# Optimization experiments

Hardware: AMD Instinct MI355X
Metric: run time of the kernel (lower is better)

Reference implementation:

```python
import jax, jax.numpy as jnp
import numpy as np

N, E, IN, HID, OUT = 40000, 640000, 128, 512, 256


def setup_inputs() -> dict:
    key = jax.random.key(0)
    ks = jax.random.split(key, 8)
    x = jax.random.normal(ks[0], (N, IN), dtype=jnp.float32)
    edge_index = jax.random.randint(ks[1], (2, E), 0, N, dtype=jnp.int64)
    # SAGEConv params: lin_l (applied to aggregated neighbors, with bias),
    # lin_r (applied to root nodes, no bias) -- PyG defaults.
    def lin(k, fin, fout):
        return jax.random.normal(k, (fin, fout), dtype=jnp.float32) / np.sqrt(fin)
    return {
        "x": x,
        "edge_index": edge_index,
        "W1l": lin(ks[2], IN, HID),
        "b1": jnp.zeros((HID,), jnp.float32),
        "W1r": lin(ks[3], IN, HID),
        "W2l": lin(ks[4], HID, OUT),
        "b2": jnp.zeros((OUT,), jnp.float32),
        "W2r": lin(ks[5], HID, OUT),
    }


def _sage_conv(x, src, dst, Wl, b, Wr):
    n = x.shape[0]
    # gather messages from source nodes, mean-aggregate at destination
    msg = x[src]                                            # [E, F]
    agg = jax.ops.segment_sum(msg, dst, num_segments=n)     # [N, F]
    cnt = jax.ops.segment_sum(jnp.ones((src.shape[0],), x.dtype), dst,
                              num_segments=n)               # [N]
    agg = agg / jnp.maximum(cnt, 1.0)[:, None]
    # out = lin_l(mean_neighbors) + lin_r(x)
    return agg @ Wl + b + x @ Wr


def reference(x, edge_index, W1l, b1, W1r, W2l, b2, W2r):
    src, dst = edge_index[0], edge_index[1]
    h = jax.nn.relu(_sage_conv(x, src, dst, W1l, b1, W1r))
    return _sage_conv(h, src, dst, W2l, b2, W2r)
```

## Files before the change

kernel.cpp:

```cpp
#include <hip/hip_runtime.h>


#define N_NODES 40000
#define N_EDGES 640000
#define F_IN 128
#define F_HID 512
#define F_OUT 256
#define NB_SCAN 157

typedef unsigned short ushort_t;
typedef __attribute__((ext_vector_type(8))) short bf16x8;
typedef __attribute__((ext_vector_type(4))) float floatx4;

__device__ __forceinline__ ushort_t f2bf(float f) {
  union { float f; unsigned int u; } x; x.f = f;
  unsigned int r = (x.u + 0x7FFFu + ((x.u >> 16) & 1u)) >> 16;
  return (ushort_t)r;
}
__device__ __forceinline__ float bf2f(ushort_t u) {
  union { unsigned int u; float f; } x; x.u = ((unsigned int)u) << 16;
  return x.f;
}

__global__ void scanA_kernel(const int* __restrict__ deg, int* __restrict__ bsum) {
  __shared__ int sdata[256];
  int i = blockIdx.x * 256 + threadIdx.x;
  sdata[threadIdx.x] = (i < N_NODES) ? deg[i] : 0;
  __syncthreads();
  #pragma unroll
  for (int off = 128; off > 0; off >>= 1) {
    if (threadIdx.x < off) sdata[threadIdx.x] += sdata[threadIdx.x + off];
    __syncthreads();
  }
  if (threadIdx.x == 0) bsum[blockIdx.x] = sdata[0];
}

__global__ void scanB_kernel(const int* __restrict__ bsum, int* __restrict__ boff) {
  __shared__ int buf[2][256];
  int tid = threadIdx.x;
  int v = (tid < NB_SCAN) ? bsum[tid] : 0;
  buf[0][tid] = v;
  __syncthreads();
  int cur = 0;
  #pragma unroll
  for (int off = 1; off < 256; off <<= 1) {
    int val = buf[cur][tid];
    if (tid >= off) val += buf[cur][tid - off];
    buf[cur ^ 1][tid] = val;
    __syncthreads();
    cur ^= 1;
  }
  if (tid < NB_SCAN) boff[tid] = buf[cur][tid] - v;
}

__global__ void scanC_kernel(const int* __restrict__ deg, const int* __restrict__ boff,
                             int* __restrict__ rowptr, int* __restrict__ cursor) {
  __shared__ int buf[2][256];
  int tid = threadIdx.x;
  int i = blockIdx.x * 256 + tid;
  int v = (i < N_NODES) ? deg[i] : 0;
  buf[0][tid] = v;
  __syncthreads();
  int cur = 0;
  #pragma unroll
  for (int off = 1; off < 256; off <<= 1) {
    int val = buf[cur][tid];
    if (tid >= off) val += buf[cur][tid - off];
    buf[cur ^ 1][tid] = val;
    __syncthreads();
    cur ^= 1;
  }
  if (i < N_NODES) {
    int ex = boff[blockIdx.x] + buf[cur][tid] - v;
    rowptr[i] = ex;
    cursor[i] = ex;
    if (i == N_NODES - 1) rowptr[N_NODES] = ex + v;
  }
}

__global__ void fill_kernel(const int* __restrict__ ei, int* __restrict__ cursor,
                            int* __restrict__ col) {
  int e = blockIdx.x * blockDim.x + threadIdx.x;
  if (e < N_EDGES) {
    int d = ei[N_EDGES + e];
    int s = ei[e];
    int pos = atomicAdd(&cursor[d], 1);
    col[pos] = s;
  }
}

__device__ __forceinline__ void wp_body(const float* __restrict__ W,
                                        ushort_t* __restrict__ Wp,
                                        int i, int K, int N, int rowoff, int koff,
                                        int KT) {
  if (i < K * N) {
    int n = i / K, k = i - n * K;
    int ng = rowoff + n, kg = koff + k;
    int gg = ng >> 6, ni = (ng >> 4) & 3, lm = ng & 15;
    int c = kg >> 3, j = kg & 7, t = c >> 2, qk = c & 3;
    size_t dst = (((size_t)(gg * (KT / 32) + t) * 4 + ni) * 64 + qk * 16 + lm) * 8 + j;
    Wp[dst] = f2bf(W[(size_t)k * N + n]);
  }
}

#define PREP_BLOCKS 9038
__global__ void prep_kernel(const float* __restrict__ x, ushort_t* __restrict__ xb,
                            const float* __restrict__ W1l, const float* __restrict__ W1r,
                            const float* __restrict__ W2l, const float* __restrict__ W2r,
                            ushort_t* __restrict__ Wp1, ushort_t* __restrict__ Wp2,
                            const float* __restrict__ b2, float* __restrict__ bc,
                            const int* __restrict__ ei, int* __restrict__ deg) {
  int b = blockIdx.x, tid = threadIdx.x;
  if (b < 5000) {
    int i = b * 256 + tid;
    const int n4 = (N_NODES * F_IN) / 4;
    if (i < n4) {
      float4 v = ((const float4*)x)[i];
      ushort4 o;
      o.x = f2bf(v.x); o.y = f2bf(v.y); o.z = f2bf(v.z); o.w = f2bf(v.w);
      ((ushort4*)xb)[i] = o;
    }
  } else if (b < 5256) {
    wp_body(W1l, Wp1, (b - 5000) * 256 + tid, 128, 512, 0, 0, 256);
  } else if (b < 5512) {
    wp_body(W1r, Wp1, (b - 5256) * 256 + tid, 128, 512, 0, 128, 256);
  } else if (b < 6024) {
    wp_body(W2l, Wp2, (b - 5512) * 256 + tid, 512, 256, 0, 0, 512);
  } else if (b < 6536) {
    wp_body(W2r, Wp2, (b - 6024) * 256 + tid, 512, 256, 256, 0, 512);
  } else if (b < 6538) {
    int i = (b - 6536) * 256 + tid;
    if (i < 512) bc[i] = (i < 256) ? 0.f : b2[i - 256];
  } else {
    int e = (b - 6538) * 256 + tid;
    if (e < N_EDGES) atomicAdd(&deg[ei[N_EDGES + e]], 1);
  }
}

__global__ void agg1_kernel(const ushort_t* __restrict__ Xb, ushort_t* __restrict__ Yb,
                            const int* __restrict__ rowptr, const int* __restrict__ colidx) {
  __shared__ int cols[64];
  int n = blockIdx.x, f = threadIdx.x;
  int s = rowptr[n], e = rowptr[n + 1];
  float s0 = 0.f, s1 = 0.f;
  for (int base = s; base < e; base += 64) {
    int cnt = min(64, e - base);
    __syncthreads();
    if (f < cnt) cols[f] = colidx[base + f];
    __syncthreads();
    int j = 0;
    for (; j + 8 <= cnt; j += 8) {
      unsigned int v[8];
      #pragma unroll
      for (int u = 0; u < 8; ++u)
        v[u] = *(const unsigned int*)(Xb + (size_t)cols[j + u] * F_IN + 2 * f);
      #pragma unroll
      for (int u = 0; u < 8; ++u) {
        s0 += bf2f((ushort_t)(v[u] & 0xffffu));
        s1 += bf2f((ushort_t)(v[u] >> 16));
      }
    }
    for (; j < cnt; ++j) {
      unsigned int v = *(const unsigned int*)(Xb + (size_t)cols[j] * F_IN + 2 * f);
      s0 += bf2f((ushort_t)(v & 0xffffu));
      s1 += bf2f((ushort_t)(v >> 16));
    }
  }
  float inv = 1.f / fmaxf((float)(e - s), 1.f);
  unsigned int o = (unsigned int)f2bf(s0 * inv) | ((unsigned int)f2bf(s1 * inv) << 16);
  *(unsigned int*)(Yb + (size_t)n * F_IN + 2 * f) = o;
}

__global__ void agg2_kernel(const ushort_t* __restrict__ hl, const float* __restrict__ hr,
                            float* __restrict__ out,
                            const int* __restrict__ rowptr, const int* __restrict__ colidx) {
  __shared__ int cols[128];
  int n = blockIdx.x, f = threadIdx.x;
  int s = rowptr[n], e = rowptr[n + 1];
  float2 hrv = *(const float2*)(hr + (size_t)n * F_OUT + 2 * f);
  float s0 = 0.f, s1 = 0.f;
  for (int base = s; base < e; base += 128) {
    int cnt = min(128, e - base);
    __syncthreads();
    if (f < cnt) cols[f] = colidx[base + f];
    __syncthreads();
    int j = 0;
    for (; j + 8 <= cnt; j += 8) {
      unsigned int v[8];
      #pragma unroll
      for (int u = 0; u < 8; ++u)
        v[u] = *(const unsigned int*)(hl + (size_t)cols[j + u] * F_OUT + 2 * f);
      #pragma unroll
      for (int u = 0; u < 8; ++u) {
        s0 += bf2f((ushort_t)(v[u] & 0xffffu));
        s1 += bf2f((ushort_t)(v[u] >> 16));
      }
    }
    for (; j < cnt; ++j) {
      unsigned int v = *(const unsigned int*)(hl + (size_t)cols[j] * F_OUT + 2 * f);
      s0 += bf2f((ushort_t)(v & 0xffffu));
      s1 += bf2f((ushort_t)(v >> 16));
    }
  }
  float inv = 1.f / fmaxf((float)(e - s), 1.f);
  float2 o;
  o.x = s0 * inv + hrv.x;
  o.y = s1 * inv + hrv.y;
  *(float2*)(out + (size_t)n * F_OUT + 2 * f) = o;
}

template <bool TWOPAIR, bool RELU, bool BIAS, bool OUT_BF16, bool SPLITOUT, int KT>
__global__ __launch_bounds__(512) void gemm_mfma(
    const ushort_t* __restrict__ A0, const ushort_t* __restrict__ A1,
    const ushort_t* __restrict__ Wp, const float* __restrict__ bias,
    float* __restrict__ Cf, ushort_t* __restrict__ Cb, int M) {
  const int KH = (KT > 256) ? 256 : KT;
  const int NH = KT / KH;
  const int NKH = KH / 8;
  __shared__ ushort_t Apan[64 * KH];
  const int tid = threadIdx.x;
  const int wave = tid >> 6, lane = tid & 63;
  const int lm = lane & 15, qk = lane >> 4;
  const int bm = blockIdx.x * 64;
  const int K0 = TWOPAIR ? KT / 2 : KT;
  const int K0c = K0 / 8;

  const ushort_t* wpg = Wp + (size_t)wave * (KT / 32) * 2048;

  auto stageA = [&](int h) {
    #pragma unroll
    for (int q = 0; q < (64 * NKH) / 512; ++q) {
      int c = tid + q * 512;
      int lc = c & (NKH - 1);
      int row = c / NKH;
      int kc = h * NKH + lc;
      const ushort_t* src = (TWOPAIR && kc >= K0c)
          ? A1 + (size_t)(bm + row) * K0 + (kc - K0c) * 8
          : A0 + (size_t)(bm + row) * K0 + kc * 8;
      bf16x8 v = *(const bf16x8*)src;
      size_t off = ((size_t)(lc * 64 + row) * 16) ^ (size_t)((lc & 7) << 4);
      *(bf16x8*)((char*)Apan + off) = v;
    }
  };

  stageA(0);
  bf16x8 bvA[4], bvB[4];
  #pragma unroll
  for (int ni = 0; ni < 4; ++ni)
    bvA[ni] = *(const bf16x8*)(wpg + (size_t)ni * 512 + lane * 8);
  __syncthreads();

  floatx4 acc[4][4] = {};
  #pragma unroll 1
  for (int h = 0; h < NH; ++h) {
    if (h) {
      __syncthreads();
      stageA(h);
      __syncthreads();
    }
    #pragma unroll 1
    for (int kb = 0; kb < KH; kb += 64) {
      const int t0 = (h * KH + kb) / 32;
      #pragma unroll
      for (int ni = 0; ni < 4; ++ni)
        bvB[ni] = *(const bf16x8*)(wpg + ((size_t)(t0 + 1) * 4 + ni) * 512 + lane * 8);

      bf16x8 av[4];
      const int kc0 = kb / 8 + qk;
      #pragma unroll
      for (int mi = 0; mi < 4; ++mi) {
        size_t off = ((size_t)(kc0 * 64 + mi * 16 + lm) * 16) ^ (size_t)((kc0 & 7) << 4);
        av[mi] = *(const bf16x8*)((char*)Apan + off);
      }
      #pragma unroll
      for (int mi = 0; mi < 4; ++mi)
        #pragma unroll
        for (int ni = 0; ni < 4; ++ni)
          acc[mi][ni] = __builtin_amdgcn_mfma_f32_16x16x32_bf16(
              bvA[ni], av[mi], acc[mi][ni], 0, 0, 0);

      if (h * KH + kb + 64 < KT) {
        #pragma unroll
        for (int ni = 0; ni < 4; ++ni)
          bvA[ni] = *(const bf16x8*)(wpg + ((size_t)(t0 + 2) * 4 + ni) * 512 + lane * 8);
      }

      const int kc1 = kb / 8 + 4 + qk;
      #pragma unroll
      for (int mi = 0; mi < 4; ++mi) {
        size_t off = ((size_t)(kc1 * 64 + mi * 16 + lm) * 16) ^ (size_t)((kc1 & 7) << 4);
        av[mi] = *(const bf16x8*)((char*)Apan + off);
      }
      #pragma unroll
      for (int mi = 0; mi < 4; ++mi)
        #pragma unroll
        for (int ni = 0; ni < 4; ++ni)
          acc[mi][ni] = __builtin_amdgcn_mfma_f32_16x16x32_bf16(
              bvB[ni], av[mi], acc[mi][ni], 0, 0, 0);
    }
  }

  #pragma unroll
  for (int ni = 0; ni < 4; ++ni) {
    int colg = wave * 64 + ni * 16 + qk * 4;
    float4 b4 = {0.f, 0.f, 0.f, 0.f};
    if (BIAS) b4 = *(const float4*)&bias[colg];
    #pragma unroll
    for (int mi = 0; mi < 4; ++mi) {
      int rowg = bm + mi * 16 + lm;
      float v0 = acc[mi][ni][0] + b4.x;
      float v1 = acc[mi][ni][1] + b4.y;
      float v2 = acc[mi][ni][2] + b4.z;
      float v3 = acc[mi][ni][3] + b4.w;
      if (RELU) {
        v0 = fmaxf(v0, 0.f); v1 = fmaxf(v1, 0.f);
        v2 = fmaxf(v2, 0.f); v3 = fmaxf(v3, 0.f);
      }
      if (SPLITOUT) {
        if (colg < 256) {
          ushort4 o = {f2bf(v0), f2bf(v1), f2bf(v2), f2bf(v3)};
          *(ushort4*)&Cb[(size_t)rowg * 256 + colg] = o;
        } else {
          float4 o = {v0, v1, v2, v3};
          *(float4*)&Cf[(size_t)rowg * 256 + (colg - 256)] = o;
        }
      } else if (OUT_BF16) {
        ushort4 o = {f2bf(v0), f2bf(v1), f2bf(v2), f2bf(v3)};
        *(ushort4*)&Cb[(size_t)rowg * 512 + colg] = o;
      } else {
        float4 o = {v0, v1, v2, v3};
        *(float4*)&Cf[(size_t)rowg * 512 + colg] = o;
      }
    }
  }
}

extern "C" void kernel_launch(void* const* d_in, const int* in_sizes, int n_in,
                              void* d_out, int out_size, void* d_ws, size_t ws_size,
                              hipStream_t stream) {
  const float* x = (const float*)d_in[0];
  const int* ei = (const int*)d_in[1];
  const float* W1l = (const float*)d_in[2];
  const float* b1 = (const float*)d_in[3];
  const float* W1r = (const float*)d_in[4];
  const float* W2l = (const float*)d_in[5];
  const float* b2 = (const float*)d_in[6];
  const float* W2r = (const float*)d_in[7];
  float* out = (float*)d_out;

  char* ws = (char*)d_ws;
  size_t off = 0;
  auto alloc = [&](size_t bytes) {
    void* p = ws + off;
    off = (off + bytes + 255) & ~(size_t)255;
    return p;
  };
  int* deg = (int*)alloc((size_t)N_NODES * 4);
  int* rowptr = (int*)alloc((size_t)(N_NODES + 1) * 4);
  int* cursor = (int*)alloc((size_t)N_NODES * 4);
  int* col = (int*)alloc((size_t)N_EDGES * 4);
  int* bsum = (int*)alloc((size_t)NB_SCAN * 4);
  int* boff = (int*)alloc((size_t)NB_SCAN * 4);
  ushort_t* x_bf = (ushort_t*)alloc((size_t)N_NODES * F_IN * 2);
  ushort_t* aggx_bf = (ushort_t*)alloc((size_t)N_NODES * F_IN * 2);
  ushort_t* h_bf = (ushort_t*)alloc((size_t)N_NODES * F_HID * 2);
  ushort_t* hl_bf = (ushort_t*)alloc((size_t)N_NODES * F_OUT * 2);
  float* hr = (float*)alloc((size_t)N_NODES * F_OUT * 4);
  ushort_t* Wp1 = (ushort_t*)alloc((size_t)512 * 256 * 2);
  ushort_t* Wp2 = (ushort_t*)alloc((size_t)512 * 512 * 2);
  float* biascat = (float*)alloc(512 * 4);

  hipMemsetAsync(deg, 0, (size_t)N_NODES * 4, stream);
  prep_kernel<<<PREP_BLOCKS, 256, 0, stream>>>(
      x, x_bf, W1l, W1r, W2l, W2r, Wp1, Wp2, b2, biascat, ei, deg);

  scanA_kernel<<<NB_SCAN, 256, 0, stream>>>(deg, bsum);
  scanB_kernel<<<1, 256, 0, stream>>>(bsum, boff);
  scanC_kernel<<<NB_SCAN, 256, 0, stream>>>(deg, boff, rowptr, cursor);
  fill_kernel<<<(N_EDGES + 255) / 256, 256, 0, stream>>>(ei, cursor, col);

  agg1_kernel<<<N_NODES, 64, 0, stream>>>(x_bf, aggx_bf, rowptr, col);
  gemm_mfma<true, true, true, true, false, 256>
      <<<625, 512, 0, stream>>>(
          aggx_bf, x_bf, Wp1, b1, nullptr, h_bf, N_NODES);

  gemm_mfma<false, false, true, false, true, 512>
      <<<625, 512, 0, stream>>>(
          h_bf, nullptr, Wp2, biascat, hr, hl_bf, N_NODES);
  agg2_kernel<<<N_NODES, 128, 0, stream>>>(hl_bf, hr, out, rowptr, col);
}
```

Measured before the change: 297.6 us.

## Halve GEMM row tile to 32 and stage full K panel at once

```diff
diff --git a/kernel.cpp b/kernel.cpp
--- a/kernel.cpp
+++ b/kernel.cpp
@@ -214,90 +214,76 @@
     const ushort_t* __restrict__ A0, const ushort_t* __restrict__ A1,
     const ushort_t* __restrict__ Wp, const float* __restrict__ bias,
     float* __restrict__ Cf, ushort_t* __restrict__ Cb, int M) {
-  const int KH = (KT > 256) ? 256 : KT;
-  const int NH = KT / KH;
-  const int NKH = KH / 8;
-  __shared__ ushort_t Apan[64 * KH];
+  const int NKC = KT / 8;
+  __shared__ ushort_t Apan[32 * KT];
   const int tid = threadIdx.x;
   const int wave = tid >> 6, lane = tid & 63;
   const int lm = lane & 15, qk = lane >> 4;
-  const int bm = blockIdx.x * 64;
+  const int bm = blockIdx.x * 32;
   const int K0 = TWOPAIR ? KT / 2 : KT;
   const int K0c = K0 / 8;
 
   const ushort_t* wpg = Wp + (size_t)wave * (KT / 32) * 2048;
 
-  auto stageA = [&](int h) {
-    #pragma unroll
-    for (int q = 0; q < (64 * NKH) / 512; ++q) {
-      int c = tid + q * 512;
-      int lc = c & (NKH - 1);
-      int row = c / NKH;
-      int kc = h * NKH + lc;
-      const ushort_t* src = (TWOPAIR && kc >= K0c)
-          ? A1 + (size_t)(bm + row) * K0 + (kc - K0c) * 8
-          : A0 + (size_t)(bm + row) * K0 + kc * 8;
-      bf16x8 v = *(const bf16x8*)src;
-      size_t off = ((size_t)(lc * 64 + row) * 16) ^ (size_t)((lc & 7) << 4);
-      *(bf16x8*)((char*)Apan + off) = v;
-    }
-  };
-
-  stageA(0);
+  #pragma unroll
+  for (int q = 0; q < (32 * NKC) / 512; ++q) {
+    int c = tid + q * 512;
+    int lc = c & (NKC - 1);
+    int row = c / NKC;
+    const ushort_t* src = (TWOPAIR && lc >= K0c)
+        ? A1 + (size_t)(bm + row) * K0 + (lc - K0c) * 8
+        : A0 + (size_t)(bm + row) * K0 + lc * 8;
+    bf16x8 v = *(const bf16x8*)src;
+    size_t off = ((size_t)(lc * 32 + row) * 16) ^ (size_t)((lc & 7) << 4);
+    *(bf16x8*)((char*)Apan + off) = v;
+  }
+
   bf16x8 bvA[4], bvB[4];
   #pragma unroll
   for (int ni = 0; ni < 4; ++ni)
     bvA[ni] = *(const bf16x8*)(wpg + (size_t)ni * 512 + lane * 8);
   __syncthreads();
 
-  floatx4 acc[4][4] = {};
+  floatx4 acc[2][4] = {};
   #pragma unroll 1
-  for (int h = 0; h < NH; ++h) {
-    if (h) {
-      __syncthreads();
-      stageA(h);
-      __syncthreads();
-    }
-    #pragma unroll 1
-    for (int kb = 0; kb < KH; kb += 64) {
-      const int t0 = (h * KH + kb) / 32;
+  for (int kb = 0; kb < KT; kb += 64) {
+    const int t0 = kb / 32;
+    #pragma unroll
+    for (int ni = 0; ni < 4; ++ni)
+      bvB[ni] = *(const bf16x8*)(wpg + ((size_t)(t0 + 1) * 4 + ni) * 512 + lane * 8);
+
+    bf16x8 av[2];
+    const int kc0 = kb / 8 + qk;
+    #pragma unroll
+    for (int mi = 0; mi < 2; ++mi) {
+      size_t off = ((size_t)(kc0 * 32 + mi * 16 + lm) * 16) ^ (size_t)((kc0 & 7) << 4);
+      av[mi] = *(const bf16x8*)((char*)Apan + off);
+    }
+    #pragma unroll
+    for (int mi = 0; mi < 2; ++mi)
       #pragma unroll
       for (int ni = 0; ni < 4; ++ni)
-        bvB[ni] = *(const bf16x8*)(wpg + ((size_t)(t0 + 1) * 4 + ni) * 512 + lane * 8);
-
-      bf16x8 av[4];
-      const int kc0 = kb / 8 + qk;
-      #pragma unroll
-      for (int mi = 0; mi < 4; ++mi) {
-        size_t off = ((size_t)(kc0 * 64 + mi * 16 + lm) * 16) ^ (size_t)((kc0 & 7) << 4);
-        av[mi] = *(const bf16x8*)((char*)Apan + off);
-      }
-      #pragma unroll
-      for (int mi = 0; mi < 4; ++mi)
-        #pragma unroll
-        for (int ni = 0; ni < 4; ++ni)
-          acc[mi][ni] = __builtin_amdgcn_mfma_f32_16x16x32_bf16(
-              bvA[ni], av[mi], acc[mi][ni], 0, 0, 0);
-
-      if (h * KH + kb + 64 < KT) {
-        #pragma unroll
-        for (int ni = 0; ni < 4; ++ni)
-          bvA[ni] = *(const bf16x8*)(wpg + ((size_t)(t0 + 2) * 4 + ni) * 512 + lane * 8);
-      }
-
-      const int kc1 = kb / 8 + 4 + qk;
-      #pragma unroll
-      for (int mi = 0; mi < 4; ++mi) {
-        size_t off = ((size_t)(kc1 * 64 + mi * 16 + lm) * 16) ^ (size_t)((kc1 & 7) << 4);
-        av[mi] = *(const bf16x8*)((char*)Apan + off);
-      }
-      #pragma unroll
-      for (int mi = 0; mi < 4; ++mi)
-        #pragma unroll
-        for (int ni = 0; ni < 4; ++ni)
-          acc[mi][ni] = __builtin_amdgcn_mfma_f32_16x16x32_bf16(
-              bvB[ni], av[mi], acc[mi][ni], 0, 0, 0);
-    }
+        acc[mi][ni] = __builtin_amdgcn_mfma_f32_16x16x32_bf16(
+            bvA[ni], av[mi], acc[mi][ni], 0, 0, 0);
+
+    if (kb + 64 < KT) {
+      #pragma unroll
+      for (int ni = 0; ni < 4; ++ni)
+        bvA[ni] = *(const bf16x8*)(wpg + ((size_t)(t0 + 2) * 4 + ni) * 512 + lane * 8);
+    }
+
+    const int kc1 = kb / 8 + 4 + qk;
+    #pragma unroll
+    for (int mi = 0; mi < 2; ++mi) {
+      size_t off = ((size_t)(kc1 * 32 + mi * 16 + lm) * 16) ^ (size_t)((kc1 & 7) << 4);
+      av[mi] = *(const bf16x8*)((char*)Apan + off);
+    }
+    #pragma unroll
+    for (int mi = 0; mi < 2; ++mi)
+      #pragma unroll
+      for (int ni = 0; ni < 4; ++ni)
+        acc[mi][ni] = __builtin_amdgcn_mfma_f32_16x16x32_bf16(
+            bvB[ni], av[mi], acc[mi][ni], 0, 0, 0);
   }
 
   #pragma unroll
@@ -306,7 +292,7 @@
     float4 b4 = {0.f, 0.f, 0.f, 0.f};
     if (BIAS) b4 = *(const float4*)&bias[colg];
     #pragma unroll
-    for (int mi = 0; mi < 4; ++mi) {
+    for (int mi = 0; mi < 2; ++mi) {
       int rowg = bm + mi * 16 + lm;
       float v0 = acc[mi][ni][0] + b4.x;
       float v1 = acc[mi][ni][1] + b4.y;
@@ -381,11 +367,11 @@
 
   agg1_kernel<<<N_NODES, 64, 0, stream>>>(x_bf, aggx_bf, rowptr, col);
   gemm_mfma<true, true, true, true, false, 256>
-      <<<625, 512, 0, stream>>>(
+      <<<1250, 512, 0, stream>>>(
           aggx_bf, x_bf, Wp1, b1, nullptr, h_bf, N_NODES);
 
   gemm_mfma<false, false, true, false, true, 512>
-      <<<625, 512, 0, stream>>>(
+      <<<1250, 512, 0, stream>>>(
           h_bf, nullptr, Wp2, biascat, hr, hl_bf, N_NODES);
   agg2_kernel<<<N_NODES, 128, 0, stream>>>(hl_bf, hr, out, rowptr, col);
 }
```

New measurement: 296.4 us. Within noise of the previous version (-0.4%).
